# Optimization experiments

Hardware: AMD Instinct MI355X
Metric: run time of the kernel (lower is better)

## Reference

```python
import jax, jax.numpy as jnp
import numpy as np

B, T, D, H, NB, K, CDIM, CTX = 8, 4096, 3, 128, 6, 20, 128, 7


def setup_inputs() -> dict:
    key = jax.random.key(0)
    ks = jax.random.split(key, 16)
    s = 0.05
    inp = {
        'p': jax.random.normal(ks[0], (B, T, D), jnp.float32),
        'W_pos': jax.random.normal(ks[1], (D, H), jnp.float32) * s,
        'b_pos': jnp.zeros((H,), jnp.float32),
        # ResnetBlockFC(2H -> H): fc_0(2H,H), fc_1(H,H), shortcut(2H,H, no bias)
        'blk_W0': jax.random.normal(ks[2], (NB, 2 * H, H), jnp.float32) * s,
        'blk_b0': jnp.zeros((NB, H), jnp.float32),
        'blk_W1': jax.random.normal(ks[3], (NB, H, H), jnp.float32) * s,
        'blk_b1': jnp.zeros((NB, H), jnp.float32),
        'blk_Ws': jax.random.normal(ks[4], (NB, 2 * H, H), jnp.float32) * s,
        # Attention: score MLP on context (dim 7 -> 1), output proj (H -> H)
        'att_Wc': jax.random.normal(ks[5], (NB, CTX, 1), jnp.float32) * s,
        'att_bc': jnp.zeros((NB, 1), jnp.float32),
        'att_Wo': jax.random.normal(ks[6], (NB, H, H), jnp.float32) * s,
        'att_bo': jnp.zeros((NB, H), jnp.float32),
        'W_c': jax.random.normal(ks[7], (H, CDIM), jnp.float32) * s,
        'b_c': jnp.zeros((CDIM,), jnp.float32),
    }
    return inp


def _knn(p):
    # squared pairwise distances [B,T,T], top-K smallest
    sq = jnp.sum(p * p, axis=-1)  # [B,T]
    d2 = sq[:, :, None] + sq[:, None, :] - 2.0 * jnp.einsum('btd,bsd->bts', p, p)
    neg, idx = jax.lax.top_k(-d2, K)            # idx: [B,T,K]
    dis = jnp.sqrt(jnp.maximum(-neg, 1e-12))    # euclidean distance [B,T,K]
    return dis, idx


def _gather(c, idx):
    # c: [B,T,h], idx: [B,T,K] -> [B,T,K,h]  (vectorized pool_local)
    return jax.vmap(lambda ci, ii: ci[ii])(c, idx)


def _resnet_block(x, W0, b0, W1, b1, Ws):
    # occupancy-networks ResnetBlockFC: shortcut(x) + fc_1(relu(fc_0(relu(x))))
    h = jnp.maximum(x, 0.0) @ W0 + b0
    dx = jnp.maximum(h, 0.0) @ W1 + b1
    return x @ Ws + dx


def reference(p, W_pos, b_pos, blk_W0, blk_b0, blk_W1, blk_b1, blk_Ws,
              att_Wc, att_bc, att_Wo, att_bo, W_c, b_c):
    dis, idx = _knn(p)
    pooled_points = _gather(p, idx)                                   # [B,T,K,3]
    p_rep = jnp.broadcast_to(p[:, :, None, :], (B, T, K, D))
    context = jnp.concatenate([dis[..., None], pooled_points, p_rep], axis=-1)  # [B,T,K,7]

    net = p @ W_pos + b_pos                                           # [B,T,H]
    last_net = jnp.zeros_like(net)
    for i in range(NB):
        pooled = _gather(net, idx)                                    # [B,T,K,H]
        # attention over the K neighbors, weights from context
        scores = context @ att_Wc[i] + att_bc[i]                      # [B,T,K,1]
        w = jax.nn.softmax(scores, axis=2)
        att = jnp.sum(w * pooled, axis=2) @ att_Wo[i] + att_bo[i]     # [B,T,H]
        x = jnp.concatenate([net, att], axis=2)                       # [B,T,2H]
        net = _resnet_block(x, blk_W0[i], blk_b0[i], blk_W1[i], blk_b1[i], blk_Ws[i])
        net = net + last_net
        last_net = net
    return net @ W_c + b_c                                            # [B,T,c_dim]
```

## Files before the change

### kernel.cpp

```cpp
#include <hip/hip_runtime.h>
#include <hip/hip_bf16.h>
#include <math.h>

#define BB 8
#define TT 4096
#define HHD 128
#define NBK 6
#define KNN 20
#define BT (BB*TT)

typedef __attribute__((ext_vector_type(8))) short bf16x8;
typedef __attribute__((ext_vector_type(4))) float f32x4;

__device__ __forceinline__ float b2f(unsigned short u){
  return __uint_as_float(((unsigned int)u) << 16);
}
__device__ __forceinline__ unsigned short f2b(float f){
  unsigned int x = __float_as_uint(f);
  unsigned int r = (x + 0x7fffu + ((x >> 16) & 1u)) >> 16;
  return (unsigned short)r;
}
__device__ __forceinline__ float ldp(const void* base, int i, int f32m){
  return f32m ? ((const float*)base)[i] : b2f(((const unsigned short*)base)[i]);
}
__device__ __forceinline__ float lo2f(unsigned int u){ return __uint_as_float(u << 16); }
__device__ __forceinline__ float hi2f(unsigned int u){ return __uint_as_float(u & 0xffff0000u); }
__device__ __forceinline__ unsigned int relu2(unsigned int u){
  unsigned int s = u & 0x80008000u;
  unsigned int m = s | (s - (s >> 15));
  return u & ~m;
}
__device__ __forceinline__ bf16x8 relu8(bf16x8 x){
  union { bf16x8 v; unsigned int u[4]; } t; t.v = x;
  t.u[0] = relu2(t.u[0]); t.u[1] = relu2(t.u[1]);
  t.u[2] = relu2(t.u[2]); t.u[3] = relu2(t.u[3]);
  return t.v;
}
__device__ __forceinline__ unsigned int splitpk(float v){
  unsigned short h = f2b(v);
  float hv = b2f(h);
  unsigned short l = f2b(v - hv);
  return (unsigned int)h | ((unsigned int)l << 16);
}

__global__ void k_detect(const unsigned short* __restrict__ wpos_raw, int* __restrict__ flag){
  int lane = threadIdx.x;
  int cnt = 0;
  for (int i = lane; i < 384; i += 64) {
    unsigned int e = (wpos_raw[i] >> 7) & 0xFFu;
    if (e >= 0x90u) cnt++;
  }
  #pragma unroll
  for (int off = 32; off > 0; off >>= 1) cnt += __shfl_down(cnt, off);
  if (lane == 0) *flag = (cnt > 10) ? 1 : 0;
}

__global__ __launch_bounds__(256) void k_prep_points(const void* __restrict__ p,
                                                     const int* __restrict__ flagp,
                                                     float4* __restrict__ pf4){
  int r = blockIdx.x*256 + threadIdx.x;
  if (r >= BT) return;
  int f32m = *flagp;
  float x = ldp(p, r*3+0, f32m), y = ldp(p, r*3+1, f32m), z = ldp(p, r*3+2, f32m);
  float sq = __fadd_rn(__fadd_rn(__fmul_rn(x,x), __fmul_rn(y,y)), __fmul_rn(z,z));
  pf4[r] = make_float4(x, y, z, sq);
}

__global__ __launch_bounds__(256) void k_net0(const float4* __restrict__ pf4,
                                              const void* __restrict__ Wpos,
                                              const void* __restrict__ bpos,
                                              const int* __restrict__ flagp,
                                              unsigned short* __restrict__ netA){
  int t = blockIdx.x*256 + threadIdx.x;
  int f32m = *flagp;
  int c = t & 127, r = t >> 7;
  float4 q = pf4[r];
  float v = ldp(bpos, c, f32m);
  v = fmaf(q.x, ldp(Wpos, c,       f32m), v);
  v = fmaf(q.y, ldp(Wpos, 128 + c, f32m), v);
  v = fmaf(q.z, ldp(Wpos, 256 + c, f32m), v);
  netA[t] = f2b(v);
}

__global__ __launch_bounds__(256) void k_transpose(const void* __restrict__ W0,
                                                   const void* __restrict__ W1,
                                                   const void* __restrict__ Ws,
                                                   const void* __restrict__ Wo,
                                                   const void* __restrict__ Wc,
                                                   const int* __restrict__ flagp,
                                                   unsigned short* __restrict__ wT){
  int t = blockIdx.x*256 + threadIdx.x;
  int f32m = *flagp;
  if (t < 196608) {
    int i = t >> 15; int rem = t & 32767; int n = rem >> 8; int k = rem & 255;
    wT[t] = f2b(ldp(W0, i*32768 + k*128 + n, f32m));
  } else if (t < 294912) {
    int u = t - 196608; int i = u >> 14; int rem = u & 16383; int n = rem >> 7; int k = rem & 127;
    wT[t] = f2b(ldp(W1, i*16384 + k*128 + n, f32m));
  } else if (t < 491520) {
    int u = t - 294912; int i = u >> 15; int rem = u & 32767; int n = rem >> 8; int k = rem & 255;
    wT[t] = f2b(ldp(Ws, i*32768 + k*128 + n, f32m));
  } else if (t < 589824) {
    int u = t - 491520; int i = u >> 14; int rem = u & 16383; int n = rem >> 7; int k = rem & 127;
    wT[t] = f2b(ldp(Wo, i*16384 + k*128 + n, f32m));
  } else if (t < 606208) {
    int u = t - 589824; int n = u >> 7; int k = u & 127;
    wT[t] = f2b(ldp(Wc, k*128 + n, f32m));
  }
}

#define INS(act, dv, iv) do { bool A_ = (act); float D_ = (dv); int I_ = (iv);        \
  _Pragma("unroll")                                                                    \
  for (int j = 19; j >= 1; --j) {                                                      \
    bool cj = A_ && (D_ < ld[j]); bool cm = A_ && (D_ < ld[j-1]);                      \
    ld[j] = cj ? (cm ? ld[j-1] : D_) : ld[j];                                          \
    li[j] = cj ? (cm ? li[j-1] : I_) : li[j];                                          \
  }                                                                                    \
  { bool c0 = A_ && (D_ < ld[0]); ld[0] = c0 ? D_ : ld[0]; li[0] = c0 ? I_ : li[0]; } \
} while(0)

#define KCAP   16
#define MARGIN 0.02f

#define KNN_FLUSH() do {                                                               \
  int mc_ = cnt;                                                                       \
  _Pragma("unroll")                                                                    \
  for (int o_ = 32; o_ > 0; o_ >>= 1) { int t_ = __shfl_xor(mc_, o_); mc_ = mc_ > t_ ? mc_ : t_; } \
  _Pragma("unroll 1")                                                                  \
  for (int u_ = 0; u_ < mc_; ++u_) {                                                   \
    float2 e_ = stk[u_*256 + tid];                                                     \
    bool act_ = u_ < cnt;                                                              \
    int piv_ = __float_as_int(e_.y);                                                   \
    float4 pp_ = tilef4[act_ ? (piv_ - ch*512) : 0];                                   \
    float dot_ = __fadd_rn(__fadd_rn(__fmul_rn(q.x,pp_.x), __fmul_rn(q.y,pp_.y)),      \
                           __fmul_rn(q.z,pp_.z));                                      \
    float d2e_ = __fsub_rn(__fadd_rn(q.w, pp_.w), __fmul_rn(2.0f, dot_));              \
    INS(act_, d2e_, piv_);                                                             \
  }                                                                                    \
  cnt = 0;                                                                             \
  atomicMin(&sthr[qlocal], __float_as_uint(fmaxf(ld[19], 0.0f)));                      \
  threshP = fminf(ld[19], __uint_as_float(sthr[qlocal])) + MARGIN;                     \
} while(0)

__global__ __launch_bounds__(256) void k_knn(const float4* __restrict__ pf4,
                                             const void* __restrict__ Wc,
                                             const void* __restrict__ bc,
                                             const int* __restrict__ flagp,
                                             unsigned short* __restrict__ idx16,
                                             unsigned short* __restrict__ wsoftb){
  __shared__ __align__(16) char smem[49152];
  __shared__ unsigned int sthr[64];
  float4* tilef4 = (float4*)smem;
  uint4*  tilesp = (uint4*)(smem + 8192);
  float2* stk    = (float2*)(smem + 16384);
  float*  lsd    = (float*)(smem + 16384);
  unsigned short* lsi16 = (unsigned short*)(smem + 36864);

  int tid  = threadIdx.x;
  int wv   = tid >> 6, lane = tid & 63;
  int cq   = lane & 15;
  int kg   = lane >> 4;
  int qlocal = wv*16 + cq;
  int b    = blockIdx.x >> 6;
  int f32m = *flagp;
  float4 q = pf4[blockIdx.x*64 + qlocal];

  if (tid < 64) sthr[tid] = 0x7F7FFFFFu;

  union FRU { bf16x8 v; unsigned int u[4]; };
  FRU bfr;
  {
    float e = (kg == 0) ? -2.0f*q.x : -2.0f*q.z;
    unsigned int ehl = splitpk(e);
    unsigned int eh = ehl & 0xffffu, el = ehl >> 16;
    float f = (kg == 0) ? -2.0f*q.y : q.w;
    unsigned int fhl = splitpk(f);
    unsigned int fh = fhl & 0xffffu, fl = fhl >> 16;
    unsigned int v0 = eh | (eh << 16);
    unsigned int v1 = el | (el << 16);
    unsigned int v2 = (kg == 0) ? (fh | (fh << 16)) : 0x3F803F80u;
    unsigned int v3 = (kg == 0) ? (fl | (fl << 16)) : fhl;
    if (kg >= 2) { v0 = 0; v1 = 0; v2 = 0; v3 = 0; }
    bfr.u[0] = v0; bfr.u[1] = v1; bfr.u[2] = v2; bfr.u[3] = v3;
  }
  const f32x4 zf = {0.f, 0.f, 0.f, 0.f};

  float ld[20]; int li[20];
  #pragma unroll
  for (int j = 0; j < 20; ++j) { ld[j] = 3.0e38f; li[j] = 0; }
  float threshP = 3.0e38f;
  int cnt = 0;

  for (int ch = 0; ch < 8; ++ch) {
    __syncthreads();
    {
      const float4* src = pf4 + (b << 12) + ch*512;
      float4 a0 = src[tid], a1 = src[tid + 256];
      tilef4[tid]       = a0;
      tilef4[tid + 256] = a1;
      tilesp[tid]       = make_uint4(splitpk(a0.x), splitpk(a0.y), splitpk(a0.z), splitpk(a0.w));
      tilesp[tid + 256] = make_uint4(splitpk(a1.x), splitpk(a1.y), splitpk(a1.z), splitpk(a1.w));
    }
    __syncthreads();
    threshP = fminf(ld[19], __uint_as_float(sthr[qlocal])) + MARGIN;
    #pragma unroll 4
    for (int g = 0; g < 32; ++g) {
      uint4 s = tilesp[g*16 + cq];
      unsigned int u0 = (kg == 0) ? s.x : s.z;
      unsigned int u2 = (kg == 0) ? s.y : s.w;
      unsigned int u3 = (kg == 0) ? u2 : 0x3F803F80u;
      if (kg >= 2) { u0 = 0; u2 = 0; u3 = 0; }
      FRU afr; afr.u[0] = u0; afr.u[1] = u0; afr.u[2] = u2; afr.u[3] = u3;
      f32x4 dd = __builtin_amdgcn_mfma_f32_16x16x32_bf16(afr.v, bfr.v, zf, 0, 0, 0);
      int pbase = ch*512 + g*16 + kg*4;
      #pragma unroll
      for (int r = 0; r < 4; ++r) {
        if (dd[r] < threshP) {
          stk[cnt*256 + tid] = make_float2(dd[r], __int_as_float(pbase + r));
          cnt++;
        }
      }
      if (__ballot(cnt >= KCAP-3)) KNN_FLUSH();
    }
    if (__ballot(cnt > 0)) KNN_FLUSH();
  }

  __syncthreads();
  #pragma unroll
  for (int j = 0; j < 20; ++j) { lsd[tid*20 + j] = ld[j]; lsi16[tid*20 + j] = (unsigned short)li[j]; }
  __syncthreads();

  if (tid < 64) {
    int w2 = tid >> 4, c2 = tid & 15;
    int base = w2*64 + c2;
    int p0 = base*20, p1 = (base+16)*20, p2 = (base+32)*20, p3 = (base+48)*20;
    int i0 = 0, i1 = 0, i2 = 0, i3 = 0;
    int rq = blockIdx.x*64 + tid;
    float4 qq = pf4[rq];
    float dis[20]; int outi[20];
    #pragma unroll
    for (int o = 0; o < 20; ++o) {
      float d0 = lsd[p0+i0], d1 = lsd[p1+i1], d2v = lsd[p2+i2], d3 = lsd[p3+i3];
      int   j0 = (int)lsi16[p0+i0], j1 = (int)lsi16[p1+i1];
      int   j2 = (int)lsi16[p2+i2], j3 = (int)lsi16[p3+i3];
      float bd = d0; int bi = j0; int sel = 0;
      if (d1  < bd || (d1  == bd && j1 < bi)) { bd = d1;  bi = j1; sel = 1; }
      if (d2v < bd || (d2v == bd && j2 < bi)) { bd = d2v; bi = j2; sel = 2; }
      if (d3  < bd || (d3  == bd && j3 < bi)) { bd = d3;  bi = j3; sel = 3; }
      i0 += (sel==0); i1 += (sel==1); i2 += (sel==2); i3 += (sel==3);
      dis[o] = sqrtf(fmaxf(bd, 1e-12f));
      outi[o] = bi;
    }
    float nx[20], ny[20], nz[20];
    #pragma unroll
    for (int k = 0; k < 20; ++k) {
      idx16[rq*20 + k] = (unsigned short)outi[k];
      float4 pp = pf4[(b << 12) + outi[k]];
      nx[k] = pp.x; ny[k] = pp.y; nz[k] = pp.z;
    }
    for (int i = 0; i < NBK; ++i) {
      float w0 = ldp(Wc,i*7+0,f32m), w1 = ldp(Wc,i*7+1,f32m), w2 = ldp(Wc,i*7+2,f32m);
      float w3 = ldp(Wc,i*7+3,f32m), w4 = ldp(Wc,i*7+4,f32m), w5 = ldp(Wc,i*7+5,f32m);
      float w6 = ldp(Wc,i*7+6,f32m);
      float bci = ldp(bc,i,f32m);
      float s[20]; float mx = -3.0e38f;
      #pragma unroll
      for (int k = 0; k < 20; ++k) {
        float v = bci;
        v = fmaf(dis[k], w0, v);
        v = fmaf(nx[k], w1, v); v = fmaf(ny[k], w2, v); v = fmaf(nz[k], w3, v);
        v = fmaf(qq.x, w4, v);  v = fmaf(qq.y, w5, v);  v = fmaf(qq.z, w6, v);
        s[k] = v; mx = fmaxf(mx, v);
      }
      float sum = 0.f;
      #pragma unroll
      for (int k = 0; k < 20; ++k) { float e = __expf(s[k] - mx); s[k] = e; sum += e; }
      float inv = 1.0f / sum;
      #pragma unroll
      for (int k = 0; k < 20; ++k) wsoftb[(rq*6 + i)*20 + k] = f2b(s[k]*inv);
    }
  }
}

__global__ __launch_bounds__(128) void k_block(const unsigned short* __restrict__ netIn,
                                               unsigned short* __restrict__ netOut,
                                               const unsigned short* __restrict__ idx16,
                                               const unsigned short* __restrict__ wsoftb,
                                               const unsigned short* __restrict__ wT,
                                               const void* __restrict__ b0s,
                                               const void* __restrict__ b1s,
                                               const void* __restrict__ bos,
                                               const int* __restrict__ flagp,
                                               int iblk, int hasResid){
  __shared__ unsigned short ldsA[16*136];
  __shared__ unsigned short ldsH[16*136];
  __shared__ float ldsF[16*132];
  int tid = threadIdx.x;
  int f32m = *flagp;
  int c = tid >> 6, lane = tid & 63;
  int b  = blockIdx.x & 7;
  int r0 = (b << 12) + ((blockIdx.x >> 3) << 4);
  const unsigned short* W0T = wT + iblk*32768;
  const unsigned short* W1T = wT + 196608 + iblk*16384;
  const unsigned short* WsT = wT + 294912 + iblk*32768;
  const unsigned short* WoT = wT + 491520 + iblk*16384;
  int m = lane & 15, qd = lane >> 4;

  {
    int r = lane >> 2, cg = lane & 3;
    int grow = r0 + r;
    int cbase = c*64 + cg*16;
    const unsigned int* ip = (const unsigned int*)(idx16 + grow*20);
    const unsigned int* wp = (const unsigned int*)(wsoftb + (grow*6 + iblk)*20);
    const unsigned short* nbase = netIn + (b << 12)*128 + cbase;
    float acc[16];
    #pragma unroll
    for (int j = 0; j < 16; ++j) acc[j] = 0.f;
    #pragma unroll 2
    for (int kk = 0; kk < 10; ++kk) {
      unsigned int pair  = ip[kk];
      unsigned int wpair = wp[kk];
      int nb0 = (int)(pair & 4095u);
      int nb1 = (int)((pair >> 16) & 4095u);
      float wk0 = lo2f(wpair);
      float wk1 = hi2f(wpair);
      const uint4* np0 = (const uint4*)(nbase + nb0*128);
      const uint4* np1 = (const uint4*)(nbase + nb1*128);
      uint4 a0 = np0[0], b0_ = np0[1];
      uint4 a1 = np1[0], b1_ = np1[1];
      acc[0]  = fmaf(wk0, lo2f(a0.x),  acc[0]);
      acc[1]  = fmaf(wk0, hi2f(a0.x),  acc[1]);
      acc[2]  = fmaf(wk0, lo2f(a0.y),  acc[2]);
      acc[3]  = fmaf(wk0, hi2f(a0.y),  acc[3]);
      acc[4]  = fmaf(wk0, lo2f(a0.z),  acc[4]);
      acc[5]  = fmaf(wk0, hi2f(a0.z),  acc[5]);
      acc[6]  = fmaf(wk0, lo2f(a0.w),  acc[6]);
      acc[7]  = fmaf(wk0, hi2f(a0.w),  acc[7]);
      acc[8]  = fmaf(wk0, lo2f(b0_.x), acc[8]);
      acc[9]  = fmaf(wk0, hi2f(b0_.x), acc[9]);
      acc[10] = fmaf(wk0, lo2f(b0_.y), acc[10]);
      acc[11] = fmaf(wk0, hi2f(b0_.y), acc[11]);
      acc[12] = fmaf(wk0, lo2f(b0_.z), acc[12]);
      acc[13] = fmaf(wk0, hi2f(b0_.z), acc[13]);
      acc[14] = fmaf(wk0, lo2f(b0_.w), acc[14]);
      acc[15] = fmaf(wk0, hi2f(b0_.w), acc[15]);
      acc[0]  = fmaf(wk1, lo2f(a1.x),  acc[0]);
      acc[1]  = fmaf(wk1, hi2f(a1.x),  acc[1]);
      acc[2]  = fmaf(wk1, lo2f(a1.y),  acc[2]);
      acc[3]  = fmaf(wk1, hi2f(a1.y),  acc[3]);
      acc[4]  = fmaf(wk1, lo2f(a1.z),  acc[4]);
      acc[5]  = fmaf(wk1, hi2f(a1.z),  acc[5]);
      acc[6]  = fmaf(wk1, lo2f(a1.w),  acc[6]);
      acc[7]  = fmaf(wk1, hi2f(a1.w),  acc[7]);
      acc[8]  = fmaf(wk1, lo2f(b1_.x), acc[8]);
      acc[9]  = fmaf(wk1, hi2f(b1_.x), acc[9]);
      acc[10] = fmaf(wk1, lo2f(b1_.y), acc[10]);
      acc[11] = fmaf(wk1, hi2f(b1_.y), acc[11]);
      acc[12] = fmaf(wk1, lo2f(b1_.z), acc[12]);
      acc[13] = fmaf(wk1, hi2f(b1_.z), acc[13]);
      acc[14] = fmaf(wk1, lo2f(b1_.w), acc[14]);
      acc[15] = fmaf(wk1, hi2f(b1_.w), acc[15]);
    }
    #pragma unroll
    for (int j = 0; j < 8; ++j) {
      unsigned int pr = ((unsigned int)f2b(acc[2*j+1]) << 16) | (unsigned int)f2b(acc[2*j]);
      *(unsigned int*)(ldsH + r*136 + cbase + 2*j) = pr;
    }
  }
  __syncthreads();

  {
    bf16x8 asf[4];
    #pragma unroll
    for (int ks = 0; ks < 4; ++ks)
      asf[ks] = *(const bf16x8*)(ldsH + m*136 + ks*32 + qd*8);
    f32x4 acc2[4];
    #pragma unroll
    for (int i = 0; i < 4; ++i) { f32x4 z = {0.f,0.f,0.f,0.f}; acc2[i] = z; }
    #pragma unroll
    for (int i = 0; i < 4; ++i) {
      int cti = c*4 + i;
      const unsigned short* bp = WoT + (cti*16 + m)*128 + qd*8;
      #pragma unroll
      for (int ks = 0; ks < 4; ++ks)
        acc2[i] = __builtin_amdgcn_mfma_f32_16x16x32_bf16(asf[ks], *(const bf16x8*)(bp + ks*32), acc2[i], 0, 0, 0);
    }
    #pragma unroll
    for (int i = 0; i < 4; ++i) {
      int col = (c*4 + i)*16 + m;
      float bo = ldp(bos, iblk*128 + col, f32m);
      #pragma unroll
      for (int rr = 0; rr < 4; ++rr)
        ldsA[(qd*4 + rr)*136 + col] = f2b(acc2[i][rr] + bo);
    }
  }
  __syncthreads();

  bf16x8 nf[4], af[4];
  {
    const unsigned short* nrow = netIn + (r0 + m)*128;
    #pragma unroll
    for (int ks = 0; ks < 4; ++ks) nf[ks] = *(const bf16x8*)(nrow + ks*32 + qd*8);
    #pragma unroll
    for (int ks = 0; ks < 4; ++ks) af[ks] = *(const bf16x8*)(ldsA + m*136 + ks*32 + qd*8);
    bf16x8 rnf[4], raf[4];
    #pragma unroll
    for (int ks = 0; ks < 4; ++ks) { rnf[ks] = relu8(nf[ks]); raf[ks] = relu8(af[ks]); }
    f32x4 acc3[4];
    #pragma unroll
    for (int i = 0; i < 4; ++i) { f32x4 z = {0.f,0.f,0.f,0.f}; acc3[i] = z; }
    #pragma unroll
    for (int i = 0; i < 4; ++i) {
      int cti = c*4 + i;
      const unsigned short* bp = W0T + (cti*16 + m)*256 + qd*8;
      #pragma unroll
      for (int ks = 0; ks < 4; ++ks)
        acc3[i] = __builtin_amdgcn_mfma_f32_16x16x32_bf16(rnf[ks], *(const bf16x8*)(bp + ks*32), acc3[i], 0, 0, 0);
      #pragma unroll
      for (int ks = 0; ks < 4; ++ks)
        acc3[i] = __builtin_amdgcn_mfma_f32_16x16x32_bf16(raf[ks], *(const bf16x8*)(bp + 128 + ks*32), acc3[i], 0, 0, 0);
    }
    #pragma unroll
    for (int i = 0; i < 4; ++i) {
      int col = (c*4 + i)*16 + m;
      float b0v = ldp(b0s, iblk*128 + col, f32m);
      #pragma unroll
      for (int rr = 0; rr < 4; ++rr)
        ldsH[(qd*4 + rr)*136 + col] = f2b(fmaxf(acc3[i][rr] + b0v, 0.f));
    }
  }
  __syncthreads();

  {
    bf16x8 hf[4];
    #pragma unroll
    for (int ks = 0; ks < 4; ++ks) hf[ks] = *(const bf16x8*)(ldsH + m*136 + ks*32 + qd*8);
    f32x4 acc4[4];
    #pragma unroll
    for (int i = 0; i < 4; ++i) { f32x4 z = {0.f,0.f,0.f,0.f}; acc4[i] = z; }
    #pragma unroll
    for (int i = 0; i < 4; ++i) {
      int cti = c*4 + i;
      const unsigned short* bp1 = W1T + (cti*16 + m)*128 + qd*8;
      #pragma unroll
      for (int ks = 0; ks < 4; ++ks)
        acc4[i] = __builtin_amdgcn_mfma_f32_16x16x32_bf16(hf[ks], *(const bf16x8*)(bp1 + ks*32), acc4[i], 0, 0, 0);
      const unsigned short* bps = WsT + (cti*16 + m)*256 + qd*8;
      #pragma unroll
      for (int ks = 0; ks < 4; ++ks)
        acc4[i] = __builtin_amdgcn_mfma_f32_16x16x32_bf16(nf[ks], *(const bf16x8*)(bps + ks*32), acc4[i], 0, 0, 0);
      #pragma unroll
      for (int ks = 0; ks < 4; ++ks)
        acc4[i] = __builtin_amdgcn_mfma_f32_16x16x32_bf16(af[ks], *(const bf16x8*)(bps + 128 + ks*32), acc4[i], 0, 0, 0);
    }
    #pragma unroll
    for (int i = 0; i < 4; ++i) {
      int col = (c*4 + i)*16 + m;
      float b1v = ldp(b1s, iblk*128 + col, f32m);
      #pragma unroll
      for (int rr = 0; rr < 4; ++rr)
        ldsF[(qd*4 + rr)*132 + col] = acc4[i][rr] + b1v;
    }
  }
  __syncthreads();

  {
    int row = tid >> 3, cg2 = tid & 7;
    int grow2 = r0 + row;
    const float* srcf = ldsF + row*132 + cg2*16;
    unsigned int outw[8];
    if (hasResid) {
      const uint4* rp = (const uint4*)(netIn + grow2*128 + cg2*16);
      uint4 ra = rp[0], rb = rp[1];
      float rs0  = lo2f(ra.x), rs1  = hi2f(ra.x), rs2  = lo2f(ra.y), rs3  = hi2f(ra.y);
      float rs4  = lo2f(ra.z), rs5  = hi2f(ra.z), rs6  = lo2f(ra.w), rs7  = hi2f(ra.w);
      float rs8  = lo2f(rb.x), rs9  = hi2f(rb.x), rs10 = lo2f(rb.y), rs11 = hi2f(rb.y);
      float rs12 = lo2f(rb.z), rs13 = hi2f(rb.z), rs14 = lo2f(rb.w), rs15 = hi2f(rb.w);
      outw[0] = (unsigned int)f2b(srcf[0]  + rs0)  | ((unsigned int)f2b(srcf[1]  + rs1)  << 16);
      outw[1] = (unsigned int)f2b(srcf[2]  + rs2)  | ((unsigned int)f2b(srcf[3]  + rs3)  << 16);
      outw[2] = (unsigned int)f2b(srcf[4]  + rs4)  | ((unsigned int)f2b(srcf[5]  + rs5)  << 16);
      outw[3] = (unsigned int)f2b(srcf[6]  + rs6)  | ((unsigned int)f2b(srcf[7]  + rs7)  << 16);
      outw[4] = (unsigned int)f2b(srcf[8]  + rs8)  | ((unsigned int)f2b(srcf[9]  + rs9)  << 16);
      outw[5] = (unsigned int)f2b(srcf[10] + rs10) | ((unsigned int)f2b(srcf[11] + rs11) << 16);
      outw[6] = (unsigned int)f2b(srcf[12] + rs12) | ((unsigned int)f2b(srcf[13] + rs13) << 16);
      outw[7] = (unsigned int)f2b(srcf[14] + rs14) | ((unsigned int)f2b(srcf[15] + rs15) << 16);
    } else {
      #pragma unroll
      for (int j = 0; j < 8; ++j)
        outw[j] = (unsigned int)f2b(srcf[2*j]) | ((unsigned int)f2b(srcf[2*j+1]) << 16);
    }
    uint4* op = (uint4*)(netOut + grow2*128 + cg2*16);
    op[0] = make_uint4(outw[0], outw[1], outw[2], outw[3]);
    op[1] = make_uint4(outw[4], outw[5], outw[6], outw[7]);
  }
}

__global__ __launch_bounds__(256) void k_final(const unsigned short* __restrict__ netIn,
                                               const unsigned short* __restrict__ WcT,
                                               const void* __restrict__ bcv,
                                               const int* __restrict__ flagp,
                                               void* __restrict__ out){
  int tid = threadIdx.x; int w = tid >> 6, lane = tid & 63;
  int f32m = *flagp;
  int t = w >> 1, c = w & 1;
  int r0 = blockIdx.x*32 + t*16;
  int m = lane & 15, qd = lane >> 4;
  bf16x8 nf[4];
  #pragma unroll
  for (int ks = 0; ks < 4; ++ks)
    nf[ks] = *(const bf16x8*)(netIn + (r0 + m)*128 + ks*32 + qd*8);
  f32x4 acc[4];
  #pragma unroll
  for (int i = 0; i < 4; ++i) { f32x4 z = {0.f,0.f,0.f,0.f}; acc[i] = z; }
  #pragma unroll
  for (int i = 0; i < 4; ++i) {
    int cti = c*4 + i;
    const unsigned short* bp = WcT + (cti*16 + m)*128 + qd*8;
    #pragma unroll
    for (int ks = 0; ks < 4; ++ks)
      acc[i] = __builtin_amdgcn_mfma_f32_16x16x32_bf16(nf[ks], *(const bf16x8*)(bp + ks*32), acc[i], 0, 0, 0);
  }
  if (f32m) {
    float* o = (float*)out;
    #pragma unroll
    for (int i = 0; i < 4; ++i) {
      int col = (c*4 + i)*16 + m;
      float bcf = ldp(bcv, col, 1);
      #pragma unroll
      for (int rr = 0; rr < 4; ++rr)
        o[(r0 + qd*4 + rr)*128 + col] = acc[i][rr] + bcf;
    }
  } else {
    unsigned short* o = (unsigned short*)out;
    #pragma unroll
    for (int i = 0; i < 4; ++i) {
      int col = (c*4 + i)*16 + m;
      float bcf = ldp(bcv, col, 0);
      #pragma unroll
      for (int rr = 0; rr < 4; ++rr)
        o[(r0 + qd*4 + rr)*128 + col] = f2b(acc[i][rr] + bcf);
    }
  }
}

extern "C" void kernel_launch(void* const* d_in, const int* in_sizes, int n_in,
                              void* d_out, int out_size, void* d_ws, size_t ws_size,
                              hipStream_t stream){
  const void* p    = d_in[0];
  const void* Wpos = d_in[1];
  const void* bpos = d_in[2];
  const void* W0   = d_in[3];
  const void* b0   = d_in[4];
  const void* W1   = d_in[5];
  const void* b1   = d_in[6];
  const void* Ws   = d_in[7];
  const void* Wc_  = d_in[8];
  const void* bc_  = d_in[9];
  const void* Wo   = d_in[10];
  const void* bo   = d_in[11];
  const void* WC   = d_in[12];
  const void* bC   = d_in[13];

  char* ws = (char*)d_ws;
  int*            flag   = (int*)(ws + 0);
  float4*         pf4    = (float4*)(ws + 256);
  unsigned short* idx16  = (unsigned short*)(ws + 524544);
  unsigned short* wsoftb = (unsigned short*)(ws + 1835264);
  unsigned short* netA   = (unsigned short*)(ws + 9699584);
  unsigned short* wT     = (unsigned short*)(ws + 18088192);

  k_detect     <<<dim3(1),     dim3(64),  0, stream>>>((const unsigned short*)Wpos, flag);
  k_prep_points<<<dim3(128),   dim3(256), 0, stream>>>(p, flag, pf4);
  k_net0       <<<dim3(16384), dim3(256), 0, stream>>>(pf4, Wpos, bpos, flag, netA);
  k_transpose  <<<dim3(2368),  dim3(256), 0, stream>>>(W0, W1, Ws, Wo, WC, flag, wT);
  k_knn        <<<dim3(512),   dim3(256), 0, stream>>>(pf4, Wc_, bc_, flag, idx16, wsoftb);

  unsigned short* a   = netA;
  unsigned short* bpt = (unsigned short*)d_out;
  for (int i = 0; i < 6; ++i) {
    k_block<<<dim3(2048), dim3(128), 0, stream>>>(a, bpt, idx16, wsoftb, wT,
                                                  b0, b1, bo, flag, i, (i > 0) ? 1 : 0);
    unsigned short* t = a; a = bpt; bpt = t;
  }
  k_final<<<dim3(1024), dim3(256), 0, stream>>>(a, wT + 589824, bC, flag, d_out);
}
```

Baseline: 608.2 us.

## Split KNN candidate scan into two halves and merge in a second kernel

The KNN kernel now scans only half of the candidate points per block, doubling the grid from 512 to 1024 blocks. Per-half top-20 lists go to scratch space in the output buffer. A new small kernel merges the two sorted lists and computes the softmax attention weights. This aims to raise occupancy and parallelism on a GPU with many CUs. In exchange it adds an extra launch, scratch traffic, and a weaker pruning threshold per half.

```diff
diff --git a/kernel.cpp b/kernel.cpp
--- a/kernel.cpp
+++ b/kernel.cpp
@@ -143,11 +143,9 @@
 } while(0)
 
 __global__ __launch_bounds__(256) void k_knn(const float4* __restrict__ pf4,
-                                             const void* __restrict__ Wc,
-                                             const void* __restrict__ bc,
                                              const int* __restrict__ flagp,
-                                             unsigned short* __restrict__ idx16,
-                                             unsigned short* __restrict__ wsoftb){
+                                             float* __restrict__ halfd,
+                                             unsigned short* __restrict__ halfi){
   __shared__ __align__(16) char smem[49152];
   __shared__ unsigned int sthr[64];
   float4* tilef4 = (float4*)smem;
@@ -161,9 +159,10 @@
   int cq   = lane & 15;
   int kg   = lane >> 4;
   int qlocal = wv*16 + cq;
-  int b    = blockIdx.x >> 6;
-  int f32m = *flagp;
-  float4 q = pf4[blockIdx.x*64 + qlocal];
+  int qg   = blockIdx.x >> 1;
+  int half = blockIdx.x & 1;
+  int b    = qg >> 6;
+  float4 q = pf4[qg*64 + qlocal];
 
   if (tid < 64) sthr[tid] = 0x7F7FFFFFu;
 
@@ -191,7 +190,7 @@
   float threshP = 3.0e38f;
   int cnt = 0;
 
-  for (int ch = 0; ch < 8; ++ch) {
+  for (int ch = half*4; ch < half*4 + 4; ++ch) {
     __syncthreads();
     {
       const float4* src = pf4 + (b << 12) + ch*512;
@@ -235,9 +234,8 @@
     int base = w2*64 + c2;
     int p0 = base*20, p1 = (base+16)*20, p2 = (base+32)*20, p3 = (base+48)*20;
     int i0 = 0, i1 = 0, i2 = 0, i3 = 0;
-    int rq = blockIdx.x*64 + tid;
-    float4 qq = pf4[rq];
-    float dis[20]; int outi[20];
+    int rq = qg*64 + tid;
+    int obase = (rq*2 + half)*20;
     #pragma unroll
     for (int o = 0; o < 20; ++o) {
       float d0 = lsd[p0+i0], d1 = lsd[p1+i1], d2v = lsd[p2+i2], d3 = lsd[p3+i3];
@@ -248,37 +246,74 @@
       if (d2v < bd || (d2v == bd && j2 < bi)) { bd = d2v; bi = j2; sel = 2; }
       if (d3  < bd || (d3  == bd && j3 < bi)) { bd = d3;  bi = j3; sel = 3; }
       i0 += (sel==0); i1 += (sel==1); i2 += (sel==2); i3 += (sel==3);
-      dis[o] = sqrtf(fmaxf(bd, 1e-12f));
-      outi[o] = bi;
-    }
-    float nx[20], ny[20], nz[20];
+      halfd[obase + o] = bd;
+      halfi[obase + o] = (unsigned short)bi;
+    }
+  }
+}
+
+__global__ __launch_bounds__(64) void k_knn2(const float4* __restrict__ pf4,
+                                             const void* __restrict__ Wc,
+                                             const void* __restrict__ bc,
+                                             const int* __restrict__ flagp,
+                                             const float* __restrict__ halfd,
+                                             const unsigned short* __restrict__ halfi,
+                                             unsigned short* __restrict__ idx16,
+                                             unsigned short* __restrict__ wsoftb){
+  int rq = blockIdx.x*64 + threadIdx.x;
+  int b  = rq >> 12;
+  int f32m = *flagp;
+  float4 qq = pf4[rq];
+
+  float h0d[20], h1d[20]; int h0i[20], h1i[20];
+  #pragma unroll
+  for (int j = 0; j < 20; ++j) {
+    h0d[j] = halfd[(rq*2 + 0)*20 + j];
+    h0i[j] = (int)halfi[(rq*2 + 0)*20 + j];
+    h1d[j] = halfd[(rq*2 + 1)*20 + j];
+    h1i[j] = (int)halfi[(rq*2 + 1)*20 + j];
+  }
+  int i0 = 0, i1 = 0;
+  float dis[20]; int outi[20];
+  #pragma unroll
+  for (int o = 0; o < 20; ++o) {
+    float d0 = h0d[i0], d1 = h1d[i1];
+    int   j0 = h0i[i0], j1 = h1i[i1];
+    bool take1 = (d1 < d0) || (d1 == d0 && j1 < j0);
+    float bd = take1 ? d1 : d0;
+    int   bi = take1 ? j1 : j0;
+    i0 += take1 ? 0 : 1;
+    i1 += take1 ? 1 : 0;
+    dis[o] = sqrtf(fmaxf(bd, 1e-12f));
+    outi[o] = bi;
+  }
+  float nx[20], ny[20], nz[20];
+  #pragma unroll
+  for (int k = 0; k < 20; ++k) {
+    idx16[rq*20 + k] = (unsigned short)outi[k];
+    float4 pp = pf4[(b << 12) + outi[k]];
+    nx[k] = pp.x; ny[k] = pp.y; nz[k] = pp.z;
+  }
+  for (int i = 0; i < NBK; ++i) {
+    float w0 = ldp(Wc,i*7+0,f32m), w1 = ldp(Wc,i*7+1,f32m), w2 = ldp(Wc,i*7+2,f32m);
+    float w3 = ldp(Wc,i*7+3,f32m), w4 = ldp(Wc,i*7+4,f32m), w5 = ldp(Wc,i*7+5,f32m);
+    float w6 = ldp(Wc,i*7+6,f32m);
+    float bci = ldp(bc,i,f32m);
+    float s[20]; float mx = -3.0e38f;
     #pragma unroll
     for (int k = 0; k < 20; ++k) {
-      idx16[rq*20 + k] = (unsigned short)outi[k];
-      float4 pp = pf4[(b << 12) + outi[k]];
-      nx[k] = pp.x; ny[k] = pp.y; nz[k] = pp.z;
-    }
-    for (int i = 0; i < NBK; ++i) {
-      float w0 = ldp(Wc,i*7+0,f32m), w1 = ldp(Wc,i*7+1,f32m), w2 = ldp(Wc,i*7+2,f32m);
-      float w3 = ldp(Wc,i*7+3,f32m), w4 = ldp(Wc,i*7+4,f32m), w5 = ldp(Wc,i*7+5,f32m);
-      float w6 = ldp(Wc,i*7+6,f32m);
-      float bci = ldp(bc,i,f32m);
-      float s[20]; float mx = -3.0e38f;
-      #pragma unroll
-      for (int k = 0; k < 20; ++k) {
-        float v = bci;
-        v = fmaf(dis[k], w0, v);
-        v = fmaf(nx[k], w1, v); v = fmaf(ny[k], w2, v); v = fmaf(nz[k], w3, v);
-        v = fmaf(qq.x, w4, v);  v = fmaf(qq.y, w5, v);  v = fmaf(qq.z, w6, v);
-        s[k] = v; mx = fmaxf(mx, v);
-      }
-      float sum = 0.f;
-      #pragma unroll
-      for (int k = 0; k < 20; ++k) { float e = __expf(s[k] - mx); s[k] = e; sum += e; }
-      float inv = 1.0f / sum;
-      #pragma unroll
-      for (int k = 0; k < 20; ++k) wsoftb[(rq*6 + i)*20 + k] = f2b(s[k]*inv);
-    }
+      float v = bci;
+      v = fmaf(dis[k], w0, v);
+      v = fmaf(nx[k], w1, v); v = fmaf(ny[k], w2, v); v = fmaf(nz[k], w3, v);
+      v = fmaf(qq.x, w4, v);  v = fmaf(qq.y, w5, v);  v = fmaf(qq.z, w6, v);
+      s[k] = v; mx = fmaxf(mx, v);
+    }
+    float sum = 0.f;
+    #pragma unroll
+    for (int k = 0; k < 20; ++k) { float e = __expf(s[k] - mx); s[k] = e; sum += e; }
+    float inv = 1.0f / sum;
+    #pragma unroll
+    for (int k = 0; k < 20; ++k) wsoftb[(rq*6 + i)*20 + k] = f2b(s[k]*inv);
   }
 }
 
@@ -569,11 +604,16 @@
   unsigned short* netA   = (unsigned short*)(ws + 9699584);
   unsigned short* wT     = (unsigned short*)(ws + 18088192);
 
+  float*          halfd  = (float*)d_out;
+  unsigned short* halfi  = (unsigned short*)((char*)d_out + 5242880);
+
   k_detect     <<<dim3(1),     dim3(64),  0, stream>>>((const unsigned short*)Wpos, flag);
   k_prep_points<<<dim3(128),   dim3(256), 0, stream>>>(p, flag, pf4);
   k_net0       <<<dim3(16384), dim3(256), 0, stream>>>(pf4, Wpos, bpos, flag, netA);
   k_transpose  <<<dim3(2368),  dim3(256), 0, stream>>>(W0, W1, Ws, Wo, WC, flag, wT);
-  k_knn        <<<dim3(512),   dim3(256), 0, stream>>>(pf4, Wc_, bc_, flag, idx16, wsoftb);
+  k_knn        <<<dim3(1024),  dim3(256), 0, stream>>>(pf4, flag, halfd, halfi);
+  k_knn2       <<<dim3(512),   dim3(64),  0, stream>>>(pf4, Wc_, bc_, flag, halfd, halfi,
+                                                       idx16, wsoftb);
 
   unsigned short* a   = netA;
   unsigned short* bpt = (unsigned short*)d_out;
```

Result: slower. 653.9 us (+7.5%).
